# Kernel tuning notes

Measured on AMD Instinct MI355X. Metric: run time of the kernel, lower is better.

Reference implementation:

```python
import jax, jax.numpy as jnp
import numpy as np

B, K, M, MN = 256, 32, 64, 256
E, H, Q = 128, 128, 128
NE, NR, NNODES = 100000, 500, 256  # entities, relations, max_nodes


def setup_inputs() -> dict:
    key = jax.random.key(0)
    ks = jax.random.split(key, 24)
    f = lambda k, s: jax.random.normal(k, s, jnp.float32) * 0.05
    inp = {}
    inp['start_entities'] = jax.random.randint(ks[0], (B,), 0, NE)
    inp['aims'] = jax.random.randint(ks[1], (B, K), 0, NE)
    inp['node_pos'] = jnp.broadcast_to(jnp.arange(1, K + 1, dtype=jnp.int32), (B, K))
    inp['neighbor_nodes'] = jax.random.randint(ks[2], (B, K, M), 0, NNODES)
    inp['neighbor_relations'] = jax.random.randint(ks[3], (B, K, M), 0, NR)
    inp['neighbors_num'] = jax.random.randint(ks[4], (B, K), 0, M + 1)
    inp['currents'] = jax.random.randint(ks[5], (B,), 0, NNODES)
    inp['candidate_nodes'] = jax.random.randint(ks[6], (B, MN), 0, NNODES)
    inp['candidate_entities'] = jax.random.randint(ks[7], (B, MN), 0, NE)
    inp['candidate_relations'] = jax.random.randint(ks[8], (B, MN), 0, NR)
    inp['candidate_masks'] = jax.random.randint(ks[9], (B, MN), 0, 2).astype(bool)
    inp['entity_emb'] = f(ks[10], (NE, E))
    inp['relation_emb'] = f(ks[11], (NR, E))
    inp['hidden_W'] = f(ks[12], (H, E)); inp['hidden_b'] = f(ks[13], (H,))
    inp['pass_W'] = f(ks[14], (H, H + E)); inp['pass_b'] = f(ks[15], (H,))
    inp['nexthop_W'] = f(ks[16], (H, H + Q)); inp['nexthop_b'] = f(ks[17], (H,))
    inp['candidate_W'] = f(ks[18], (H, H + 2 * E)); inp['candidate_b'] = f(ks[19], (H,))
    inp['gate_W'] = f(ks[20], (1, H + Q)); inp['gate_b'] = f(ks[21], (1,))
    inp['query'] = f(ks[22], (B, Q))
    return inp


def _linear(x, W, b):
    return x @ W.T + b


def _lrelu(x):
    return jax.nn.leaky_relu(x, 0.01)  # torch LeakyReLU default


def _gather_nodes(node_emb, idx):
    # node_emb: (B, N+2, H), idx: (B, ...) -> (B, ..., H)
    b = node_emb.shape[0]
    g = jnp.take_along_axis(node_emb, idx.reshape(b, -1)[:, :, None], axis=1)
    return g.reshape(*idx.shape, node_emb.shape[-1])


def reference(start_entities, aims, node_pos, neighbor_nodes, neighbor_relations,
              neighbors_num, currents, candidate_nodes, candidate_entities,
              candidate_relations, candidate_masks, entity_emb, relation_emb,
              hidden_W, hidden_b, pass_W, pass_b, nexthop_W, nexthop_b,
              candidate_W, candidate_b, gate_W, gate_b, query):
    # ---- Agent.init ----
    node_emb = jnp.zeros((B, NNODES + 2, H), jnp.float32)
    init = _lrelu(_linear(entity_emb[start_entities], hidden_W, hidden_b))
    node_emb = node_emb.at[:, 0].set(init)
    # ---- Agent.aggregate: gather -> Linear -> masked mean -> scatter ----
    aim_e = entity_emb[aims]                                   # (B,K,E)
    nb_node = _gather_nodes(node_emb, neighbor_nodes)          # (B,K,M,H)
    nb_rel = relation_emb[neighbor_relations]                  # (B,K,M,E)
    nb = _linear(jnp.concatenate([nb_node, nb_rel], -1), pass_W, pass_b)  # pass_activation = identity
    keep = jnp.arange(M) < neighbors_num[:, :, None]           # (B,K,M)
    nb = jnp.where(keep[..., None], nb, 0.0)
    denom = (neighbors_num + (neighbors_num == 0)).astype(jnp.float32)
    agg = nb.sum(axis=2) / denom[..., None]                    # (B,K,H)
    upd = _lrelu(_linear(aim_e, hidden_W, hidden_b) + agg)
    node_emb = node_emb.at[jnp.arange(B)[:, None], node_pos].set(upd)
    # ---- Agent.next_hop ----
    cur = _gather_nodes(node_emb, currents)                    # (B,H)
    cur_cat = jnp.concatenate([cur, query], axis=1)            # (B,H+Q)
    state = _lrelu(_linear(cur_cat, nexthop_W, nexthop_b))     # (B,H)
    cnode = _gather_nodes(node_emb, candidate_nodes)           # (B,MN,H)
    cand = _lrelu(_linear(jnp.concatenate(
        [cnode, entity_emb[candidate_entities], relation_emb[candidate_relations]], -1),
        candidate_W, candidate_b))                             # (B,MN,H)
    thresh = _linear(cur_cat, gate_W, gate_b)                  # (B,1)
    scores = jnp.einsum('bh,bmh->bm', state, cand) / jnp.sqrt(jnp.float32(E))
    scores = jnp.where(candidate_masks, scores, jnp.float32(-100000.0))
    final_scores = jnp.concatenate([scores, thresh], axis=1)   # (B,MN+1)
    return final_scores
```

## Files before the change

### kernel.cpp

```cpp
#include <hip/hip_runtime.h>

#define B 256
#define K 32
#define M 64
#define MN 256
#define E 128
#define H 128
#define Q 128
#define NSLOT 258
#define CTILE 32
#define XPAD 392

typedef __attribute__((ext_vector_type(8))) short short8;
typedef __attribute__((ext_vector_type(4))) short short4b;
typedef __attribute__((ext_vector_type(4))) float f32x4;

__device__ __forceinline__ float lrelu(float x){ return x >= 0.f ? x : 0.01f*x; }

__device__ __forceinline__ unsigned short f2bf(float f){
    unsigned int u = __float_as_uint(f);
    unsigned int r = u + 0x7FFFu + ((u >> 16) & 1u);
    return (unsigned short)(r >> 16);
}

__device__ __forceinline__ short4b pack4(float4 v){
    short4b r;
    r.x = (short)f2bf(v.x); r.y = (short)f2bf(v.y);
    r.z = (short)f2bf(v.z); r.w = (short)f2bf(v.w);
    return r;
}

__global__ void k_front(const int* __restrict__ aims, const int* __restrict__ nbr_nodes,
                        const int* __restrict__ nbr_rels, const int* __restrict__ nbr_num,
                        const int* __restrict__ start_ent, const int* __restrict__ node_pos,
                        const float* __restrict__ ent_emb, const float* __restrict__ rel_emb,
                        const float* __restrict__ hW, const float* __restrict__ hb,
                        const float* __restrict__ passW, const float* __restrict__ candW,
                        unsigned short* __restrict__ Xg, float* __restrict__ ab,
                        int* __restrict__ map,
                        float* __restrict__ init_out, float* __restrict__ wninit_out,
                        unsigned short* __restrict__ Wf, unsigned short* __restrict__ Wcatf){
    int blk = blockIdx.x, t = threadIdx.x;
    __shared__ float e[128];
    __shared__ float si[128];

    if (blk >= 832) {
        int w = t >> 6, lane = t & 63;
        int bk = (blk - 832)*4 + w;
        int num = nbr_num[bk];
        int sidx = nbr_rels[(long)bk*M + lane];
        int nn   = nbr_nodes[(long)bk*M + lane];
        unsigned long long mask = __ballot((lane < num) && (nn == 0));
        int c0 = (int)__popcll(mask);
        float denom = (float)(num > 0 ? num : 1);
        float ax = 0.f, ay = 0.f;
        int m = 0;
        for (; m + 8 <= num; m += 8) {
            int r0 = __shfl(sidx, m+0), r1 = __shfl(sidx, m+1);
            int r2 = __shfl(sidx, m+2), r3 = __shfl(sidx, m+3);
            int r4 = __shfl(sidx, m+4), r5 = __shfl(sidx, m+5);
            int r6 = __shfl(sidx, m+6), r7 = __shfl(sidx, m+7);
            float2 v0 = *(const float2*)&rel_emb[(long)r0*E + lane*2];
            float2 v1 = *(const float2*)&rel_emb[(long)r1*E + lane*2];
            float2 v2 = *(const float2*)&rel_emb[(long)r2*E + lane*2];
            float2 v3 = *(const float2*)&rel_emb[(long)r3*E + lane*2];
            float2 v4 = *(const float2*)&rel_emb[(long)r4*E + lane*2];
            float2 v5 = *(const float2*)&rel_emb[(long)r5*E + lane*2];
            float2 v6 = *(const float2*)&rel_emb[(long)r6*E + lane*2];
            float2 v7 = *(const float2*)&rel_emb[(long)r7*E + lane*2];
            ax += (v0.x + v1.x) + (v2.x + v3.x) + (v4.x + v5.x) + (v6.x + v7.x);
            ay += (v0.y + v1.y) + (v2.y + v3.y) + (v4.y + v5.y) + (v6.y + v7.y);
        }
        for (; m < num; ++m) {
            int r = __shfl(sidx, m);
            float2 v = *(const float2*)&rel_emb[(long)r*E + lane*2];
            ax += v.x; ay += v.y;
        }
        ushort2 rp; rp.x = f2bf(ax/denom); rp.y = f2bf(ay/denom);
        *(ushort2*)&Xg[(long)bk*256 + lane*2] = rp;
        float2 av = *(const float2*)&ent_emb[(long)aims[bk]*E + lane*2];
        ushort2 apk; apk.x = f2bf(av.x); apk.y = f2bf(av.y);
        *(ushort2*)&Xg[(long)bk*256 + 128 + lane*2] = apk;
        if (lane == 0) {
            ab[bk*2+0] = (float)c0 / denom;
            ab[bk*2+1] = (float)num / denom;
        }
        return;
    }

    int pb = blk;
    if (pb < 256) {
        int b = pb;
        if (t < 128) e[t] = ent_emb[(long)start_ent[b]*E + t];
        __syncthreads();
        if (t < 128) {
            float acc = hb[t];
            #pragma unroll 8
            for (int j=0;j<E;j++) acc += hW[t*E+j]*e[j];
            float v = lrelu(acc);
            si[t] = v;
            init_out[b*H+t] = v;
        }
        __syncthreads();
        if (t < 128) {
            float acc2 = 0.f;
            #pragma unroll 8
            for (int j=0;j<H;j++) acc2 += passW[t*(H+E)+j]*si[j];
            wninit_out[b*H+t] = acc2;
        }
    } else if (pb < 512) {
        int b = pb - 256;
        for (int i=t;i<NSLOT;i+=256) map[b*NSLOT+i] = -2;
        __syncthreads();
        if (t==0) map[b*NSLOT+0] = -1;
        __syncthreads();
        if (t<K) map[b*NSLOT + node_pos[b*K+t]] = t;
    } else if (pb < 704) {
        int i = (pb-512)*256 + t;
        int j = i & 7;
        int l = (i >> 3) & 63;
        int ct = (i >> 9) & 1;
        int r = i >> 10;
        int ks = r % 12, w = r / 12;
        int row = w*32 + ct*16 + (l & 15);
        int col = ks*32 + (l >> 4)*8 + j;
        Wf[i] = f2bf(candW[row*384 + col]);
    } else {
        int i = (pb-704)*256 + t;
        int j = i & 7;
        int l = (i >> 3) & 63;
        int ct = (i >> 9) & 1;
        int r = i >> 10;
        int ks = r & 7, w = r >> 3;
        int row = w*32 + ct*16 + (l & 15);
        int col = ks*32 + (l >> 4)*8 + j;
        float v = (col < 128) ? passW[row*256 + 128 + col] : hW[row*128 + (col-128)];
        Wcatf[i] = f2bf(v);
    }
}

__global__ void k_updg(const unsigned short* __restrict__ Xg, const float* __restrict__ ab,
                       const unsigned short* __restrict__ Wcatf,
                       const float* __restrict__ hb_, const float* __restrict__ passb,
                       const float* __restrict__ wninit,
                       const int* __restrict__ currents, const int* __restrict__ map,
                       const float* __restrict__ init, const float* __restrict__ query,
                       const float* __restrict__ nW, const float* __restrict__ nb_,
                       const float* __restrict__ gW, const float* __restrict__ gb,
                       float* __restrict__ upd, float* __restrict__ state,
                       float* __restrict__ out){
    int b = blockIdx.x;
    int t = threadIdx.x;
    __shared__ __align__(16) unsigned short Xs[32][264];
    __shared__ float wni[128];
    __shared__ float sab[64];
    __shared__ float cc[H+Q];
    __shared__ float wsum[2];
    #pragma unroll
    for (int it = 0; it < 4; it++) {
        int idx = it*256 + t;
        int r = idx >> 5;
        int cg = (idx & 31) * 8;
        *(short8*)&Xs[r][cg] = *(const short8*)&Xg[((long)b*32 + r)*256 + cg];
    }
    if (t < 128) wni[t] = wninit[b*128 + t];
    else if (t < 192) sab[t-128] = ab[b*64 + (t-128)];

    int w    = t >> 6;
    int lane = t & 63;
    int l16  = lane & 15;
    int lhi  = lane >> 4;
    int hbase = w*32;

    short8 bw[8][2];
    #pragma unroll
    for (int ks = 0; ks < 8; ks++) {
        #pragma unroll
        for (int ct = 0; ct < 2; ct++)
            bw[ks][ct] = *(const short8*)&Wcatf[((((w*8+ks)*2+ct)*64) + lane)*8];
    }
    int mvc = map[b*NSLOT + currents[b]];
    __syncthreads();

    f32x4 acc[2][2];
    #pragma unroll
    for (int rt=0;rt<2;rt++)
        #pragma unroll
        for (int ct=0;ct<2;ct++)
            acc[rt][ct] = (f32x4){0.f,0.f,0.f,0.f};

    #pragma unroll
    for (int ks = 0; ks < 8; ks++) {
        int kof = ks*32 + lhi*8;
        short8 a0 = *(const short8*)&Xs[l16][kof];
        short8 a1 = *(const short8*)&Xs[16 + l16][kof];
        acc[0][0] = __builtin_amdgcn_mfma_f32_16x16x32_bf16(a0, bw[ks][0], acc[0][0], 0, 0, 0);
        acc[0][1] = __builtin_amdgcn_mfma_f32_16x16x32_bf16(a0, bw[ks][1], acc[0][1], 0, 0, 0);
        acc[1][0] = __builtin_amdgcn_mfma_f32_16x16x32_bf16(a1, bw[ks][0], acc[1][0], 0, 0, 0);
        acc[1][1] = __builtin_amdgcn_mfma_f32_16x16x32_bf16(a1, bw[ks][1], acc[1][1], 0, 0, 0);
    }

    int h0 = hbase + l16, h1 = hbase + 16 + l16;
    float hb0 = hb_[h0], hb1 = hb_[h1];
    float pb0 = passb[h0], pb1 = passb[h1];
    float w0 = wni[h0],  w1 = wni[h1];

    if (t < 128) {
        cc[t] = (mvc == -1) ? init[b*H + t] : 0.f;
        cc[H+t] = query[b*Q + t];
    }

    float uv[2][2][4];
    #pragma unroll
    for (int rt=0; rt<2; rt++) {
        #pragma unroll
        for (int i=0;i<4;i++) {
            int r = rt*16 + 4*lhi + i;
            float al = sab[r*2], be = sab[r*2+1];
            float v0 = lrelu(hb0 + al*w0 + be*pb0 + acc[rt][0][i]);
            float v1 = lrelu(hb1 + al*w1 + be*pb1 + acc[rt][1][i]);
            uv[rt][0][i] = v0; uv[rt][1][i] = v1;
            upd[((long)b*32 + r)*128 + h0] = v0;
            upd[((long)b*32 + r)*128 + h1] = v1;
        }
    }
    __syncthreads();
    if (mvc >= 0) {
        #pragma unroll
        for (int rt=0; rt<2; rt++) {
            #pragma unroll
            for (int i=0;i<4;i++) {
                int r = rt*16 + 4*lhi + i;
                if (r == mvc) { cc[h0] = uv[rt][0][i]; cc[h1] = uv[rt][1][i]; }
            }
        }
    }
    __syncthreads();

    if (t < 128) {
        float sacc = nb_[t];
        #pragma unroll 8
        for (int j=0;j<H+Q;j++) sacc += nW[t*(H+Q)+j]*cc[j];
        state[b*H+t] = lrelu(sacc);
        float tv = gW[t]*cc[t] + gW[H+t]*cc[H+t];
        for (int off=32; off>0; off>>=1) tv += __shfl_down(tv, off);
        if ((t&63)==0) wsum[t>>6] = tv;
    }
    __syncthreads();
    if (t==0) out[b*(MN+1) + MN] = wsum[0] + wsum[1] + gb[0];
}

__global__ __launch_bounds__(256, 2)
void k_cand(const int* __restrict__ cnodes, const int* __restrict__ cents,
            const int* __restrict__ crels, const int* __restrict__ cmask,
            const int* __restrict__ map,
            const float* __restrict__ init, const float* __restrict__ upd,
            const float* __restrict__ ent_emb, const float* __restrict__ rel_emb,
            const unsigned short* __restrict__ Wf, const float* __restrict__ cb,
            const float* __restrict__ state,
            float* __restrict__ out){
    int blk = blockIdx.x;
    int b  = blk >> 1;
    int cbase = (blk & 1) * 128;
    int t  = threadIdx.x;

    __shared__ __align__(16) unsigned short Xb[CTILE][XPAD];
    __shared__ float sscore[4][CTILE];
    __shared__ int sce[128], scr[128], smv[128];

    if (t < 128) {
        int row = b*MN + cbase + t;
        sce[t] = cents[row];
        scr[t] = crels[row];
        smv[t] = map[b*NSLOT + cnodes[row]];
    }

    int w    = t >> 6;
    int lane = t & 63;
    int l16  = lane & 15;
    int lhi  = lane >> 4;
    int c8   = t >> 5;
    int q    = t & 31;

    short8 bw[12][2];
    #pragma unroll
    for (int ks = 0; ks < 12; ks++) {
        #pragma unroll
        for (int ct = 0; ct < 2; ct++)
            bw[ks][ct] = *(const short8*)&Wf[((((w*12+ks)*2+ct)*64) + lane)*8];
    }
    float s0  = state[b*H + w*32 + l16];
    float s1  = state[b*H + w*32 + 16 + l16];
    float cb0 = cb[w*32 + l16];
    float cb1 = cb[w*32 + 16 + l16];
    __syncthreads();

    #pragma unroll
    for (int tile = 0; tile < 4; ++tile) {
        #pragma unroll
        for (int i = 0; i < 4; i++) {
            int ci = tile*32 + i*8 + c8;
            int cl = i*8 + c8;
            int mv = smv[ci];
            float4 nv = {0.f,0.f,0.f,0.f};
            if (mv == -1)      nv = *(const float4*)&init[b*H + q*4];
            else if (mv >= 0)  nv = *(const float4*)&upd[((long)b*K+mv)*H + q*4];
            float4 ev = *(const float4*)&ent_emb[(long)sce[ci]*E + q*4];
            float4 rv = *(const float4*)&rel_emb[(long)scr[ci]*E + q*4];
            *(short4b*)&Xb[cl][q*4]       = pack4(nv);
            *(short4b*)&Xb[cl][128 + q*4] = pack4(ev);
            *(short4b*)&Xb[cl][256 + q*4] = pack4(rv);
        }
        __syncthreads();

        f32x4 acc[2][2];
        #pragma unroll
        for (int rt=0;rt<2;rt++)
            #pragma unroll
            for (int ct=0;ct<2;ct++)
                acc[rt][ct] = (f32x4){0.f,0.f,0.f,0.f};

        #pragma unroll
        for (int ks = 0; ks < 12; ks++) {
            int kof = ks*32 + lhi*8;
            short8 a0 = *(const short8*)&Xb[l16][kof];
            short8 a1 = *(const short8*)&Xb[16 + l16][kof];
            acc[0][0] = __builtin_amdgcn_mfma_f32_16x16x32_bf16(a0, bw[ks][0], acc[0][0], 0, 0, 0);
            acc[0][1] = __builtin_amdgcn_mfma_f32_16x16x32_bf16(a0, bw[ks][1], acc[0][1], 0, 0, 0);
            acc[1][0] = __builtin_amdgcn_mfma_f32_16x16x32_bf16(a1, bw[ks][0], acc[1][0], 0, 0, 0);
            acc[1][1] = __builtin_amdgcn_mfma_f32_16x16x32_bf16(a1, bw[ks][1], acc[1][1], 0, 0, 0);
        }

        #pragma unroll
        for (int rt=0; rt<2; rt++) {
            float ps[4];
            #pragma unroll
            for (int i=0;i<4;i++)
                ps[i] = lrelu(acc[rt][0][i] + cb0)*s0 + lrelu(acc[rt][1][i] + cb1)*s1;
            #pragma unroll
            for (int msk=1; msk<16; msk<<=1) {
                #pragma unroll
                for (int i=0;i<4;i++) ps[i] += __shfl_xor(ps[i], msk);
            }
            if (l16 == 0) {
                #pragma unroll
                for (int i=0;i<4;i++)
                    sscore[w][rt*16 + 4*lhi + i] = ps[i];
            }
        }
        __syncthreads();

        if (t < CTILE) {
            int row = b*MN + cbase + tile*32 + t;
            float s = (sscore[0][t] + sscore[1][t] + sscore[2][t] + sscore[3][t])
                      * 0.08838834764831845f;
            out[b*(MN+1) + cbase + tile*32 + t] = cmask[row] ? s : -100000.0f;
        }
    }
}

extern "C" void kernel_launch(void* const* d_in, const int* in_sizes, int n_in,
                              void* d_out, int out_size, void* d_ws, size_t ws_size,
                              hipStream_t stream){
    (void)in_sizes; (void)n_in; (void)out_size; (void)ws_size;
    const int* start_entities      = (const int*)d_in[0];
    const int* aims                = (const int*)d_in[1];
    const int* node_pos            = (const int*)d_in[2];
    const int* neighbor_nodes      = (const int*)d_in[3];
    const int* neighbor_relations  = (const int*)d_in[4];
    const int* neighbors_num       = (const int*)d_in[5];
    const int* currents            = (const int*)d_in[6];
    const int* candidate_nodes     = (const int*)d_in[7];
    const int* candidate_entities  = (const int*)d_in[8];
    const int* candidate_relations = (const int*)d_in[9];
    const int* candidate_masks     = (const int*)d_in[10];
    const float* entity_emb   = (const float*)d_in[11];
    const float* relation_emb = (const float*)d_in[12];
    const float* hidden_W     = (const float*)d_in[13];
    const float* hidden_b     = (const float*)d_in[14];
    const float* pass_W       = (const float*)d_in[15];
    const float* pass_b       = (const float*)d_in[16];
    const float* nexthop_W    = (const float*)d_in[17];
    const float* nexthop_b    = (const float*)d_in[18];
    const float* candidate_W  = (const float*)d_in[19];
    const float* candidate_b  = (const float*)d_in[20];
    const float* gate_W       = (const float*)d_in[21];
    const float* gate_b       = (const float*)d_in[22];
    const float* query        = (const float*)d_in[23];
    float* out = (float*)d_out;

    float* ws     = (float*)d_ws;
    float* init   = ws;
    float* wninit = init + B*H;
    float* upd    = wninit + B*H;
    float* state  = upd + (long)B*K*H;
    float* ab     = state + B*H;
    int*   map    = (int*)(ab + B*K*2);
    unsigned short* Wf    = (unsigned short*)(map + B*NSLOT);
    unsigned short* Wcatf = Wf + 49152;
    unsigned short* Xg    = Wcatf + 32768;

    k_front<<<832 + (B*K)/4, 256, 0, stream>>>(aims, neighbor_nodes, neighbor_relations,
                                               neighbors_num, start_entities, node_pos,
                                               entity_emb, relation_emb,
                                               hidden_W, hidden_b, pass_W, candidate_W,
                                               Xg, ab, map, init, wninit, Wf, Wcatf);
    k_updg<<<B, 256, 0, stream>>>(Xg, ab, Wcatf, hidden_b, pass_b, wninit,
                                  currents, map, init, query,
                                  nexthop_W, nexthop_b, gate_W, gate_b,
                                  upd, state, out);
    k_cand<<<2*B, 256, 0, stream>>>(candidate_nodes, candidate_entities,
                                    candidate_relations, candidate_masks,
                                    map, init, upd, entity_emb, relation_emb,
                                    Wf, candidate_b, state, out);
}
```

Measured before the change: 54.61 us.

## Replace relation-embedding gather-sum with histogram times precomputed relation-projection matmul

```diff
diff --git a/kernel.cpp b/kernel.cpp
--- a/kernel.cpp
+++ b/kernel.cpp
@@ -30,60 +30,58 @@
     return r;
 }
 
+__device__ __forceinline__ short8 f8_from(const float* __restrict__ p){
+    float4 u = *(const float4*)p;
+    float4 v = *(const float4*)(p + 4);
+    short8 s;
+    s[0]=(short)f2bf(u.x); s[1]=(short)f2bf(u.y); s[2]=(short)f2bf(u.z); s[3]=(short)f2bf(u.w);
+    s[4]=(short)f2bf(v.x); s[5]=(short)f2bf(v.y); s[6]=(short)f2bf(v.z); s[7]=(short)f2bf(v.w);
+    return s;
+}
+
 __global__ void k_front(const int* __restrict__ aims, const int* __restrict__ nbr_nodes,
                         const int* __restrict__ nbr_rels, const int* __restrict__ nbr_num,
                         const int* __restrict__ start_ent, const int* __restrict__ node_pos,
                         const float* __restrict__ ent_emb, const float* __restrict__ rel_emb,
                         const float* __restrict__ hW, const float* __restrict__ hb,
                         const float* __restrict__ passW, const float* __restrict__ candW,
-                        unsigned short* __restrict__ Xg, float* __restrict__ ab,
-                        int* __restrict__ map,
+                        float* __restrict__ ab, int* __restrict__ map,
                         float* __restrict__ init_out, float* __restrict__ wninit_out,
-                        unsigned short* __restrict__ Wf, unsigned short* __restrict__ Wcatf){
+                        unsigned short* __restrict__ Wf, unsigned short* __restrict__ Wcatf,
+                        unsigned short* __restrict__ Pf,
+                        unsigned short* __restrict__ XhG, unsigned short* __restrict__ XaG){
     int blk = blockIdx.x, t = threadIdx.x;
     __shared__ float e[128];
     __shared__ float si[128];
-
-    if (blk >= 832) {
+    __shared__ unsigned int hist[4][512];
+    __shared__ float sden[4];
+
+    if (blk >= 848) {
+        int hb4 = blk - 848;
+        for (int i = t; i < 2048; i += 256) ((unsigned int*)hist)[i] = 0u;
+        __syncthreads();
         int w = t >> 6, lane = t & 63;
-        int bk = (blk - 832)*4 + w;
+        int bk = hb4*4 + w;
         int num = nbr_num[bk];
-        int sidx = nbr_rels[(long)bk*M + lane];
-        int nn   = nbr_nodes[(long)bk*M + lane];
+        int nr  = nbr_rels[(long)bk*M + lane];
+        int nn  = nbr_nodes[(long)bk*M + lane];
         unsigned long long mask = __ballot((lane < num) && (nn == 0));
         int c0 = (int)__popcll(mask);
         float denom = (float)(num > 0 ? num : 1);
-        float ax = 0.f, ay = 0.f;
-        int m = 0;
-        for (; m + 8 <= num; m += 8) {
-            int r0 = __shfl(sidx, m+0), r1 = __shfl(sidx, m+1);
-            int r2 = __shfl(sidx, m+2), r3 = __shfl(sidx, m+3);
-            int r4 = __shfl(sidx, m+4), r5 = __shfl(sidx, m+5);
-            int r6 = __shfl(sidx, m+6), r7 = __shfl(sidx, m+7);
-            float2 v0 = *(const float2*)&rel_emb[(long)r0*E + lane*2];
-            float2 v1 = *(const float2*)&rel_emb[(long)r1*E + lane*2];
-            float2 v2 = *(const float2*)&rel_emb[(long)r2*E + lane*2];
-            float2 v3 = *(const float2*)&rel_emb[(long)r3*E + lane*2];
-            float2 v4 = *(const float2*)&rel_emb[(long)r4*E + lane*2];
-            float2 v5 = *(const float2*)&rel_emb[(long)r5*E + lane*2];
-            float2 v6 = *(const float2*)&rel_emb[(long)r6*E + lane*2];
-            float2 v7 = *(const float2*)&rel_emb[(long)r7*E + lane*2];
-            ax += (v0.x + v1.x) + (v2.x + v3.x) + (v4.x + v5.x) + (v6.x + v7.x);
-            ay += (v0.y + v1.y) + (v2.y + v3.y) + (v4.y + v5.y) + (v6.y + v7.y);
-        }
-        for (; m < num; ++m) {
-            int r = __shfl(sidx, m);
-            float2 v = *(const float2*)&rel_emb[(long)r*E + lane*2];
-            ax += v.x; ay += v.y;
-        }
-        ushort2 rp; rp.x = f2bf(ax/denom); rp.y = f2bf(ay/denom);
-        *(ushort2*)&Xg[(long)bk*256 + lane*2] = rp;
+        if (lane < num) atomicAdd(&hist[w][nr], 1u);
         float2 av = *(const float2*)&ent_emb[(long)aims[bk]*E + lane*2];
-        ushort2 apk; apk.x = f2bf(av.x); apk.y = f2bf(av.y);
-        *(ushort2*)&Xg[(long)bk*256 + 128 + lane*2] = apk;
+        ushort2 ap; ap.x = f2bf(av.x); ap.y = f2bf(av.y);
+        *(ushort2*)&XaG[(long)bk*128 + lane*2] = ap;
         if (lane == 0) {
             ab[bk*2+0] = (float)c0 / denom;
             ab[bk*2+1] = (float)num / denom;
+            sden[w] = 1.f / denom;
+        }
+        __syncthreads();
+        for (int i = t; i < 2048; i += 256) {
+            int w2 = i >> 9, r = i & 511;
+            float v = (float)hist[w2][r] * sden[w2];
+            XhG[((long)(hb4*4 + w2))*512 + r] = f2bf(v);
         }
         return;
     }
@@ -125,7 +123,7 @@
         int row = w*32 + ct*16 + (l & 15);
         int col = ks*32 + (l >> 4)*8 + j;
         Wf[i] = f2bf(candW[row*384 + col]);
-    } else {
+    } else if (pb < 832) {
         int i = (pb-704)*256 + t;
         int j = i & 7;
         int l = (i >> 3) & 63;
@@ -136,11 +134,51 @@
         int col = ks*32 + (l >> 4)*8 + j;
         float v = (col < 128) ? passW[row*256 + 128 + col] : hW[row*128 + (col-128)];
         Wcatf[i] = f2bf(v);
-    }
-}
-
-__global__ void k_updg(const unsigned short* __restrict__ Xg, const float* __restrict__ ab,
+    } else {
+        int g = pb - 832;
+        int w = t >> 6, lane = t & 63;
+        int l16 = lane & 15, lhi = lane >> 4;
+        int hbase = w*32;
+        const short8 z8 = (short8){0,0,0,0,0,0,0,0};
+        f32x4 acc[2][2];
+        #pragma unroll
+        for (int rt=0;rt<2;rt++)
+            #pragma unroll
+            for (int ct=0;ct<2;ct++)
+                acc[rt][ct] = (f32x4){0.f,0.f,0.f,0.f};
+        #pragma unroll
+        for (int ks2 = 0; ks2 < 4; ks2++) {
+            int kof = ks2*32 + lhi*8;
+            int r0 = g*32 + l16, r1 = g*32 + 16 + l16;
+            short8 a0 = (r0 < 500) ? f8_from(&rel_emb[(long)r0*E + kof]) : z8;
+            short8 a1 = (r1 < 500) ? f8_from(&rel_emb[(long)r1*E + kof]) : z8;
+            short8 b0 = f8_from(&passW[(long)(hbase + l16)*(H+E) + H + kof]);
+            short8 b1 = f8_from(&passW[(long)(hbase + 16 + l16)*(H+E) + H + kof]);
+            acc[0][0] = __builtin_amdgcn_mfma_f32_16x16x32_bf16(a0, b0, acc[0][0], 0, 0, 0);
+            acc[0][1] = __builtin_amdgcn_mfma_f32_16x16x32_bf16(a0, b1, acc[0][1], 0, 0, 0);
+            acc[1][0] = __builtin_amdgcn_mfma_f32_16x16x32_bf16(a1, b0, acc[1][0], 0, 0, 0);
+            acc[1][1] = __builtin_amdgcn_mfma_f32_16x16x32_bf16(a1, b1, acc[1][1], 0, 0, 0);
+        }
+        #pragma unroll
+        for (int rt=0; rt<2; rt++) {
+            #pragma unroll
+            for (int ct=0; ct<2; ct++) {
+                #pragma unroll
+                for (int i=0;i<4;i++) {
+                    int rp = rt*16 + 4*lhi + i;
+                    long idx = ((long)((w*16 + g)*2 + ct))*512 + (l16 + (rp>>3)*16)*8 + (rp & 7);
+                    Pf[idx] = f2bf(acc[rt][ct][i]);
+                }
+            }
+        }
+    }
+}
+
+__global__ void k_updg(const unsigned short* __restrict__ XhG,
+                       const unsigned short* __restrict__ XaG,
+                       const float* __restrict__ ab,
                        const unsigned short* __restrict__ Wcatf,
+                       const unsigned short* __restrict__ Pf,
                        const float* __restrict__ hb_, const float* __restrict__ passb,
                        const float* __restrict__ wninit,
                        const int* __restrict__ currents, const int* __restrict__ map,
@@ -151,17 +189,25 @@
                        float* __restrict__ out){
     int b = blockIdx.x;
     int t = threadIdx.x;
-    __shared__ __align__(16) unsigned short Xs[32][264];
+    __shared__ __align__(16) unsigned short Xh[32][520];
+    __shared__ __align__(16) unsigned short Xa[32][136];
     __shared__ float wni[128];
     __shared__ float sab[64];
     __shared__ float cc[H+Q];
     __shared__ float wsum[2];
     #pragma unroll
-    for (int it = 0; it < 4; it++) {
+    for (int it = 0; it < 8; it++) {
         int idx = it*256 + t;
-        int r = idx >> 5;
-        int cg = (idx & 31) * 8;
-        *(short8*)&Xs[r][cg] = *(const short8*)&Xg[((long)b*32 + r)*256 + cg];
+        int r = idx >> 6;
+        int cg = (idx & 63) * 8;
+        *(short8*)&Xh[r][cg] = *(const short8*)&XhG[((long)b*32 + r)*512 + cg];
+    }
+    #pragma unroll
+    for (int it = 0; it < 2; it++) {
+        int idx = it*256 + t;
+        int r = idx >> 4;
+        int cg = (idx & 15) * 8;
+        *(short8*)&Xa[r][cg] = *(const short8*)&XaG[((long)b*32 + r)*128 + cg];
     }
     if (t < 128) wni[t] = wninit[b*128 + t];
     else if (t < 192) sab[t-128] = ab[b*64 + (t-128)];
@@ -171,14 +217,6 @@
     int l16  = lane & 15;
     int lhi  = lane >> 4;
     int hbase = w*32;
-
-    short8 bw[8][2];
-    #pragma unroll
-    for (int ks = 0; ks < 8; ks++) {
-        #pragma unroll
-        for (int ct = 0; ct < 2; ct++)
-            bw[ks][ct] = *(const short8*)&Wcatf[((((w*8+ks)*2+ct)*64) + lane)*8];
-    }
     int mvc = map[b*NSLOT + currents[b]];
     __syncthreads();
 
@@ -189,15 +227,29 @@
         for (int ct=0;ct<2;ct++)
             acc[rt][ct] = (f32x4){0.f,0.f,0.f,0.f};
 
-    #pragma unroll
-    for (int ks = 0; ks < 8; ks++) {
+    #pragma unroll 4
+    for (int ks = 0; ks < 16; ks++) {
         int kof = ks*32 + lhi*8;
-        short8 a0 = *(const short8*)&Xs[l16][kof];
-        short8 a1 = *(const short8*)&Xs[16 + l16][kof];
-        acc[0][0] = __builtin_amdgcn_mfma_f32_16x16x32_bf16(a0, bw[ks][0], acc[0][0], 0, 0, 0);
-        acc[0][1] = __builtin_amdgcn_mfma_f32_16x16x32_bf16(a0, bw[ks][1], acc[0][1], 0, 0, 0);
-        acc[1][0] = __builtin_amdgcn_mfma_f32_16x16x32_bf16(a1, bw[ks][0], acc[1][0], 0, 0, 0);
-        acc[1][1] = __builtin_amdgcn_mfma_f32_16x16x32_bf16(a1, bw[ks][1], acc[1][1], 0, 0, 0);
+        short8 a0 = *(const short8*)&Xh[l16][kof];
+        short8 a1 = *(const short8*)&Xh[16 + l16][kof];
+        short8 b0 = *(const short8*)&Pf[(((long)(w*16+ks)*2 + 0)*64 + lane)*8];
+        short8 b1 = *(const short8*)&Pf[(((long)(w*16+ks)*2 + 1)*64 + lane)*8];
+        acc[0][0] = __builtin_amdgcn_mfma_f32_16x16x32_bf16(a0, b0, acc[0][0], 0, 0, 0);
+        acc[0][1] = __builtin_amdgcn_mfma_f32_16x16x32_bf16(a0, b1, acc[0][1], 0, 0, 0);
+        acc[1][0] = __builtin_amdgcn_mfma_f32_16x16x32_bf16(a1, b0, acc[1][0], 0, 0, 0);
+        acc[1][1] = __builtin_amdgcn_mfma_f32_16x16x32_bf16(a1, b1, acc[1][1], 0, 0, 0);
+    }
+    #pragma unroll
+    for (int ks2 = 0; ks2 < 4; ks2++) {
+        int kof = ks2*32 + lhi*8;
+        short8 a0 = *(const short8*)&Xa[l16][kof];
+        short8 a1 = *(const short8*)&Xa[16 + l16][kof];
+        short8 b0 = *(const short8*)&Wcatf[((((w*8 + 4 + ks2)*2 + 0)*64) + lane)*8];
+        short8 b1 = *(const short8*)&Wcatf[((((w*8 + 4 + ks2)*2 + 1)*64) + lane)*8];
+        acc[0][0] = __builtin_amdgcn_mfma_f32_16x16x32_bf16(a0, b0, acc[0][0], 0, 0, 0);
+        acc[0][1] = __builtin_amdgcn_mfma_f32_16x16x32_bf16(a0, b1, acc[0][1], 0, 0, 0);
+        acc[1][0] = __builtin_amdgcn_mfma_f32_16x16x32_bf16(a1, b0, acc[1][0], 0, 0, 0);
+        acc[1][1] = __builtin_amdgcn_mfma_f32_16x16x32_bf16(a1, b1, acc[1][1], 0, 0, 0);
     }
 
     int h0 = hbase + l16, h1 = hbase + 16 + l16;
@@ -398,14 +450,17 @@
     int*   map    = (int*)(ab + B*K*2);
     unsigned short* Wf    = (unsigned short*)(map + B*NSLOT);
     unsigned short* Wcatf = Wf + 49152;
-    unsigned short* Xg    = Wcatf + 32768;
-
-    k_front<<<832 + (B*K)/4, 256, 0, stream>>>(aims, neighbor_nodes, neighbor_relations,
+    unsigned short* Pf    = Wcatf + 32768;
+    unsigned short* XhG   = Pf + 65536;
+    unsigned short* XaG   = XhG + (long)B*K*512;
+
+    k_front<<<848 + (B*K)/4, 256, 0, stream>>>(aims, neighbor_nodes, neighbor_relations,
                                                neighbors_num, start_entities, node_pos,
                                                entity_emb, relation_emb,
                                                hidden_W, hidden_b, pass_W, candidate_W,
-                                               Xg, ab, map, init, wninit, Wf, Wcatf);
-    k_updg<<<B, 256, 0, stream>>>(Xg, ab, Wcatf, hidden_b, pass_b, wninit,
+                                               ab, map, init, wninit, Wf, Wcatf,
+                                               Pf, XhG, XaG);
+    k_updg<<<B, 256, 0, stream>>>(XhG, XaG, ab, Wcatf, Pf, hidden_b, pass_b, wninit,
                                   currents, map, init, query,
                                   nexthop_W, nexthop_b, gate_W, gate_b,
                                   upd, state, out);
```

Measured after the change: 54.07 us. About the same (-1.0%).
